# Kernel optimization log

Hardware: AMD Instinct MI355X
Metric: run time of the kernel (lower is better)

Reference implementation:

```python
import jax, jax.numpy as jnp
import numpy as np
from jax import lax

NUM_HEADS = 8
EPS = 1e-12  # torch F.normalize eps


def setup_inputs() -> dict:
    key = jax.random.key(0)
    ks = jax.random.split(key, 5)
    dim = 192
    b, h, w = 8, 128, 128
    return {
        "x": jax.random.normal(ks[0], (b, dim, h, w), jnp.float32),
        "w_qkv": jax.random.normal(ks[1], (3 * dim, dim, 1, 1), jnp.float32) * (1.0 / np.sqrt(dim)),
        "w_dw": jax.random.normal(ks[2], (3 * dim, 1, 3, 3), jnp.float32) * (1.0 / 3.0),
        "w_proj": jax.random.normal(ks[3], (dim, dim, 1, 1), jnp.float32) * (1.0 / np.sqrt(dim)),
        "temperature": jnp.ones((NUM_HEADS, 1, 1), jnp.float32),
    }


def _l2norm(t):
    n = jnp.sqrt(jnp.sum(t * t, axis=-1, keepdims=True))
    return t / jnp.maximum(n, EPS)


def reference(x, w_qkv, w_dw, w_proj, temperature):
    b, c, h, w = x.shape
    # 1x1 conv to 3*dim channels
    qkv = jnp.einsum('bchw,oc->bohw', x, w_qkv[:, :, 0, 0])
    # depthwise 3x3 conv, dilation=2, padding=2, groups=3*dim
    qkv = lax.conv_general_dilated(
        qkv, w_dw, window_strides=(1, 1), padding=((2, 2), (2, 2)),
        rhs_dilation=(2, 2), feature_group_count=3 * c,
        dimension_numbers=('NCHW', 'OIHW', 'NCHW'))
    q, k, v = jnp.split(qkv, 3, axis=1)
    ch = c // NUM_HEADS
    def heads(t):  # b (head ch) h w -> b head ch (h w)
        return t.reshape(b, NUM_HEADS, ch, h * w)
    q, k, v = heads(q), heads(k), heads(v)
    q = _l2norm(q)
    k = _l2norm(k)
    attn = jnp.einsum('bhcn,bhdn->bhcd', q, k) * temperature  # (b, head, ch, ch)
    attn = jax.nn.softmax(attn, axis=-1)
    out = jnp.einsum('bhcd,bhdn->bhcn', attn, v)
    out = out.reshape(b, c, h, w)
    out = jnp.einsum('bchw,oc->bohw', out, w_proj[:, :, 0, 0])
    return out
```

## Files before the change

### kernel.cpp

```cpp
#include <hip/hip_runtime.h>


#define DIM 192
#define NH 8
#define CH 24
#define IH 128
#define IW 128
#define NPIX (IH*IW)
#define BATCH 8
#define QKVC (3*DIM)
#define PAD 200
#define SPAD 264

typedef unsigned short u16;
typedef short bf16x8 __attribute__((ext_vector_type(8)));
typedef float f32x4 __attribute__((ext_vector_type(4)));

__device__ __forceinline__ float b2f(u16 u){
    unsigned v = ((unsigned)u) << 16;
    return __builtin_bit_cast(float, v);
}
__device__ __forceinline__ u16 f2b(float f){
    unsigned u = __builtin_bit_cast(unsigned, f);
    u += 0x7fffu + ((u >> 16) & 1u);
    return (u16)(u >> 16);
}

__device__ __forceinline__ void conv_row8(const u16* __restrict__ rp, int px0,
        float w0, float w1, float w2, float* o_){
    float f[12];
    if(px0 > 0){
        unsigned u = *(const unsigned*)(rp + px0 - 2);
        f[0] = b2f((u16)u); f[1] = b2f((u16)(u >> 16));
    } else { f[0] = 0.f; f[1] = 0.f; }
    bf16x8 v = *(const bf16x8*)(rp + px0);
    #pragma unroll
    for(int j=0;j<8;j++) f[2+j] = b2f((u16)v[j]);
    if(px0 < 120){
        unsigned u = *(const unsigned*)(rp + px0 + 8);
        f[10] = b2f((u16)u); f[11] = b2f((u16)(u >> 16));
    } else { f[10] = 0.f; f[11] = 0.f; }
    #pragma unroll
    for(int i=0;i<8;i++) o_[i] += w0*f[i] + w1*f[i+2] + w2*f[i+4];
}

__global__ __launch_bounds__(256) void k0_wcvt(const float* __restrict__ wqkv,
        u16* __restrict__ wb){
    int i = (blockIdx.x*256 + threadIdx.x)*4;
    f32x4 v = *(const f32x4*)&wqkv[i];
    unsigned lo = ((unsigned)f2b(v[1]) << 16) | f2b(v[0]);
    unsigned hi = ((unsigned)f2b(v[3]) << 16) | f2b(v[2]);
    *(uint2*)&wb[i] = make_uint2(lo, hi);
}

__global__ __launch_bounds__(256) void k1_qkv(const float* __restrict__ x,
        const u16* __restrict__ wb, u16* __restrict__ qkv_pre){
    __shared__ __align__(16) u16 Xl[64*PAD];
    const int tid = threadIdx.x;
    const int pt = blockIdx.x, b = blockIdx.y;
    const int p0 = pt*64;
    {
        const int px = tid & 63, grp = tid >> 6;
        const float* xb = x + (size_t)b*DIM*NPIX + p0 + px;
        #pragma unroll
        for(int cg = 0; cg < 6; cg++){
            int cb = grp*48 + cg*8;
            bf16x8 v;
            #pragma unroll
            for(int j=0;j<8;j++) v[j] = (short)f2b(xb[(size_t)(cb+j)*NPIX]);
            *(bf16x8*)&Xl[px*PAD + cb] = v;
        }
    }
    __syncthreads();
    const int lane = tid & 63, w = tid >> 6;
    const int r = lane & 15, quad = lane >> 4;
    u16* op = qkv_pre + (size_t)b*QKVC*NPIX + p0;
    for(int i = 0; i < 9; i++){
        const int ob = (w*9 + i)*16;
        f32x4 acc[4];
        { f32x4 z = {0.f,0.f,0.f,0.f}; for(int j=0;j<4;j++) acc[j]=z; }
        const u16* wp = wb + (size_t)(ob + r)*DIM;
        #pragma unroll
        for(int kk = 0; kk < 6; kk++){
            const int k0 = kk*32 + quad*8;
            bf16x8 a0 = *(const bf16x8*)&wp[k0];
            #pragma unroll
            for(int ni=0; ni<4; ni++){
                bf16x8 bb = *(const bf16x8*)&Xl[(ni*16 + r)*PAD + k0];
                acc[ni] = __builtin_amdgcn_mfma_f32_16x16x32_bf16(bb, a0, acc[ni], 0,0,0);
            }
        }
        #pragma unroll
        for(int ni=0; ni<4; ni++){
            int o = ob + r;
            int px = ni*16 + quad*4;
            f32x4 a = acc[ni];
            unsigned lo = ((unsigned)f2b(a[1]) << 16) | f2b(a[0]);
            unsigned hi = ((unsigned)f2b(a[3]) << 16) | f2b(a[2]);
            *(uint2*)&op[(size_t)o*NPIX + px] = make_uint2(lo, hi);
        }
    }
}

__global__ __launch_bounds__(256) void k2_gram(const u16* __restrict__ qkv_pre,
        const float* __restrict__ wdw, float* __restrict__ G){
    __shared__ __align__(16) u16 Sl[48*SPAD];
    const int tid = threadIdx.x;
    const int pc = blockIdx.x, h = blockIdx.y, b = blockIdx.z;
    const int lane = tid & 63, w = tid >> 6;
    const int r = lane & 15, quad = lane >> 4;
    f32x4 acc[6];
    { f32x4 z = {0.f,0.f,0.f,0.f}; for(int i=0;i<6;i++) acc[i]=z; }
    for(int chunk = 0; chunk < 2; chunk++){
        if(chunk) __syncthreads();
        for(int it = 0; it < 6; it++){
            int t = tid + it*256;
            int c48 = t >> 5, oct = t & 31;
            int isK = (c48 >= CH);
            int c = isK ? (c48 - CH) : c48;
            int ch = (isK ? DIM : 0) + h*CH + c;
            const u16* base = qkv_pre + ((size_t)b*QKVC + ch)*NPIX;
            const float* wv = wdw + ch*9;
            int py = pc*4 + chunk*2 + (oct >> 4);
            int px0 = (oct & 15)*8;
            float o_[8];
            #pragma unroll
            for(int i=0;i<8;i++) o_[i]=0.f;
            #pragma unroll
            for(int ky=0;ky<3;ky++){
                int ry = py + 2*ky - 2;
                if(ry < 0 || ry >= IH) continue;
                conv_row8(base + ry*IW, px0, wv[ky*3], wv[ky*3+1], wv[ky*3+2], o_);
            }
            bf16x8 v;
            #pragma unroll
            for(int i=0;i<8;i++) v[i] = (short)f2b(o_[i]);
            *(bf16x8*)&Sl[c48*SPAD + oct*8] = v;
        }
        __syncthreads();
        #pragma unroll
        for(int kk = 0; kk < 2; kk++){
            const int k0 = w*64 + kk*32 + quad*8;
            bf16x8 f0 = *(const bf16x8*)&Sl[(     r)*SPAD + k0];
            bf16x8 f1 = *(const bf16x8*)&Sl[(16 + r)*SPAD + k0];
            bf16x8 f2 = *(const bf16x8*)&Sl[(32 + r)*SPAD + k0];
            acc[0] = __builtin_amdgcn_mfma_f32_16x16x32_bf16(f0, f0, acc[0], 0,0,0);
            acc[1] = __builtin_amdgcn_mfma_f32_16x16x32_bf16(f0, f1, acc[1], 0,0,0);
            acc[2] = __builtin_amdgcn_mfma_f32_16x16x32_bf16(f0, f2, acc[2], 0,0,0);
            acc[3] = __builtin_amdgcn_mfma_f32_16x16x32_bf16(f1, f1, acc[3], 0,0,0);
            acc[4] = __builtin_amdgcn_mfma_f32_16x16x32_bf16(f1, f2, acc[4], 0,0,0);
            acc[5] = __builtin_amdgcn_mfma_f32_16x16x32_bf16(f2, f2, acc[5], 0,0,0);
        }
    }
    __syncthreads();
    float* R = (float*)Sl;
    #pragma unroll
    for(int tile=0; tile<6; tile++)
        *(f32x4*)&R[(w*6 + tile)*256 + lane*4] = acc[tile];
    __syncthreads();
    float* Gb = G + (size_t)(b*NH + h)*48*48;
    #pragma unroll
    for(int i=0; i<6; i++){
        int idx = tid + i*256;
        int tile = idx >> 8, rem = idx & 255;
        int ln = rem >> 2, t = rem & 3;
        float s = R[idx] + R[1536 + idx] + R[2*1536 + idx] + R[3*1536 + idx];
        int ti = (tile<3) ? 0 : ((tile<5) ? 1 : 2);
        int tj = (tile<3) ? tile : ((tile<5) ? (tile-2) : 2);
        int c = ti*16 + (ln >> 4)*4 + t;
        int d = tj*16 + (ln & 15);
        atomicAdd(&Gb[c*48 + d], s);
    }
}

__global__ __launch_bounds__(256) void k3_attn(const float* __restrict__ G,
        const float* __restrict__ temp, const float* __restrict__ wproj,
        u16* __restrict__ M){
    __shared__ float attn[NH][CH][CH];
    __shared__ float nq[DIM], nk[DIM];
    const int b = blockIdx.x, tid = threadIdx.x;
    const float* Gb = G + (size_t)b*NH*48*48;
    if(tid < DIM){
        int h = tid / CH, c = tid % CH;
        const float* g = Gb + (size_t)h*48*48;
        nq[tid] = fmaxf(sqrtf(g[c*48 + c]), 1e-12f);
        nk[tid] = fmaxf(sqrtf(g[(CH+c)*48 + (CH+c)]), 1e-12f);
    }
    __syncthreads();
    if(tid < DIM){
        int h = tid / CH, c = tid % CH;
        float t = temp[h];
        const float* g = Gb + (size_t)h*48*48 + c*48 + CH;
        float row[CH];
        float mx = -1e30f;
        #pragma unroll
        for(int d=0; d<CH; d++){
            float v = g[d] / (nq[tid]*nk[h*CH+d]) * t;
            row[d]=v; mx = fmaxf(mx,v);
        }
        float sum=0.f;
        #pragma unroll
        for(int d=0;d<CH;d++){ row[d]=expf(row[d]-mx); sum+=row[d]; }
        float inv = 1.f/sum;
        #pragma unroll
        for(int d=0;d<CH;d++) attn[h][c][d] = row[d]*inv;
    }
    __syncthreads();
    u16* Mb = M + (size_t)b*DIM*DIM;
    for(int i = tid; i < DIM*DIM; i += 256){
        int o = i / DIM, hd = i % DIM;
        int h = hd / CH, d = hd % CH;
        float s = 0.f;
        #pragma unroll
        for(int c=0;c<CH;c++)
            s += wproj[o*DIM + h*CH + c] * attn[h][c][d];
        Mb[i] = f2b(s);
    }
}

__global__ __launch_bounds__(256) void k45_out(const u16* __restrict__ qkv_pre,
        const float* __restrict__ wdw, const u16* __restrict__ M,
        float* __restrict__ out){
    __shared__ __align__(16) u16 Vt[64*PAD];
    const int tid = threadIdx.x;
    const int half = blockIdx.x & 1, py = blockIdx.x >> 1, b = blockIdx.y;
    const int p0 = py*IW + half*64;
    for(int it = 0; it < 3; it++){
        int t = tid + it*256;
        int chp = t >> 3, oct = t & 7;
        int px0g = half*64 + oct*8;
        float oo[2][8];
        #pragma unroll
        for(int j=0;j<2;j++){
            int ch = 2*chp + j;
            const u16* base = qkv_pre + ((size_t)b*QKVC + 2*DIM + ch)*NPIX;
            const float* wv = wdw + (2*DIM + ch)*9;
            #pragma unroll
            for(int i=0;i<8;i++) oo[j][i]=0.f;
            #pragma unroll
            for(int ky=0;ky<3;ky++){
                int ry = py + 2*ky - 2;
                if(ry < 0 || ry >= IH) continue;
                conv_row8(base + ry*IW, px0g, wv[ky*3], wv[ky*3+1], wv[ky*3+2], oo[j]);
            }
        }
        #pragma unroll
        for(int i=0;i<8;i++){
            unsigned pk = (unsigned)f2b(oo[0][i]) | ((unsigned)f2b(oo[1][i]) << 16);
            *(unsigned*)&Vt[(oct*8+i)*PAD + 2*chp] = pk;
        }
    }
    __syncthreads();
    const int lane = tid & 63, w = tid >> 6;
    const int r = lane & 15, quad = lane >> 4;
    const u16* Mb = M + (size_t)b*DIM*DIM;
    float* op = out + (size_t)b*DIM*NPIX + p0;
    for(int i = 0; i < 3; i++){
        const int ob = (w*3 + i)*16;
        f32x4 acc[4];
        { f32x4 z = {0.f,0.f,0.f,0.f}; for(int j=0;j<4;j++) acc[j]=z; }
        const u16* mp = Mb + (size_t)(ob + r)*DIM;
        #pragma unroll
        for(int kk = 0; kk < 6; kk++){
            const int k0 = kk*32 + quad*8;
            bf16x8 a0 = *(const bf16x8*)&mp[k0];
            #pragma unroll
            for(int ni=0; ni<4; ni++){
                bf16x8 bb = *(const bf16x8*)&Vt[(ni*16 + r)*PAD + k0];
                acc[ni] = __builtin_amdgcn_mfma_f32_16x16x32_bf16(bb, a0, acc[ni], 0,0,0);
            }
        }
        #pragma unroll
        for(int ni=0; ni<4; ni++)
            *(f32x4*)&op[(size_t)(ob + r)*NPIX + ni*16 + quad*4] = acc[ni];
    }
}

extern "C" void kernel_launch(void* const* d_in, const int* in_sizes, int n_in,
                              void* d_out, int out_size, void* d_ws, size_t ws_size,
                              hipStream_t stream){
    const float* x     = (const float*)d_in[0];
    const float* wqkv  = (const float*)d_in[1];
    const float* wdw   = (const float*)d_in[2];
    const float* wproj = (const float*)d_in[3];
    const float* temp  = (const float*)d_in[4];
    float* out = (float*)d_out;

    char* ws = (char*)d_ws;
    u16* qkv_pre = (u16*)ws;
    size_t off = (size_t)BATCH*QKVC*NPIX*sizeof(u16);
    float* G  = (float*)(ws + off); off += (size_t)BATCH*NH*48*48*4;
    u16* M    = (u16*)(ws + off);   off += (size_t)BATCH*DIM*DIM*2;
    u16* wb   = (u16*)(ws + off);   off += (size_t)QKVC*DIM*2;

    hipMemsetAsync(G, 0, (size_t)BATCH*NH*48*48*sizeof(float), stream);

    k0_wcvt<<<108, 256, 0, stream>>>(wqkv, wb);
    k1_qkv <<<dim3(256, BATCH), 256, 0, stream>>>(x, wb, qkv_pre);
    k2_gram<<<dim3(32, NH, BATCH), 256, 0, stream>>>(qkv_pre, wdw, G);
    k3_attn<<<BATCH, 256, 0, stream>>>(G, temp, wproj, M);
    k45_out<<<dim3(256, BATCH), 256, 0, stream>>>(qkv_pre, wdw, M, out);
}
```

Measured before the change: 446.6 us.

## Process four rows per output block with register-resident M and remapped blocks

The output kernel now runs 64 blocks per batch instead of 256, and each block loops over four image rows for one half-width. The projection matrix M fragments are loaded into registers once and reused across those rows, which removes the repeated global loads of M. Block indices in both the gram and output kernels are remapped so that neighbouring blocks work on interleaved row strips, which may change how L2 is shared between concurrent blocks. The trade-off is fewer blocks in flight (512 total on a large GPU), higher register pressure from the 18 held fragments, and a barrier for each row.

```diff
diff --git a/kernel.cpp b/kernel.cpp
--- a/kernel.cpp
+++ b/kernel.cpp
@@ -106,7 +106,8 @@
         const float* __restrict__ wdw, float* __restrict__ G){
     __shared__ __align__(16) u16 Sl[48*SPAD];
     const int tid = threadIdx.x;
-    const int pc = blockIdx.x, h = blockIdx.y, b = blockIdx.z;
+    const int bx = blockIdx.x, h = blockIdx.y, b = blockIdx.z;
+    const int pc = 4*(bx & 7) + (bx >> 3);
     const int lane = tid & 63, w = tid >> 6;
     const int r = lane & 15, quad = lane >> 4;
     f32x4 acc[6];
@@ -223,56 +224,71 @@
         float* __restrict__ out){
     __shared__ __align__(16) u16 Vt[64*PAD];
     const int tid = threadIdx.x;
-    const int half = blockIdx.x & 1, py = blockIdx.x >> 1, b = blockIdx.y;
-    const int p0 = py*IW + half*64;
-    for(int it = 0; it < 3; it++){
-        int t = tid + it*256;
-        int chp = t >> 3, oct = t & 7;
-        int px0g = half*64 + oct*8;
-        float oo[2][8];
-        #pragma unroll
-        for(int j=0;j<2;j++){
-            int ch = 2*chp + j;
-            const u16* base = qkv_pre + ((size_t)b*QKVC + 2*DIM + ch)*NPIX;
-            const float* wv = wdw + (2*DIM + ch)*9;
-            #pragma unroll
-            for(int i=0;i<8;i++) oo[j][i]=0.f;
-            #pragma unroll
-            for(int ky=0;ky<3;ky++){
-                int ry = py + 2*ky - 2;
-                if(ry < 0 || ry >= IH) continue;
-                conv_row8(base + ry*IW, px0g, wv[ky*3], wv[ky*3+1], wv[ky*3+2], oo[j]);
-            }
-        }
-        #pragma unroll
-        for(int i=0;i<8;i++){
-            unsigned pk = (unsigned)f2b(oo[0][i]) | ((unsigned)f2b(oo[1][i]) << 16);
-            *(unsigned*)&Vt[(oct*8+i)*PAD + 2*chp] = pk;
-        }
-    }
-    __syncthreads();
+    const int bx = blockIdx.x, b = blockIdx.y;
+    const int strip = 4*(bx & 7) + (bx >> 4);
+    const int half  = (bx >> 3) & 1;
+    const int r0 = strip*4;
     const int lane = tid & 63, w = tid >> 6;
     const int r = lane & 15, quad = lane >> 4;
-    const u16* Mb = M + (size_t)b*DIM*DIM;
-    float* op = out + (size_t)b*DIM*NPIX + p0;
-    for(int i = 0; i < 3; i++){
-        const int ob = (w*3 + i)*16;
-        f32x4 acc[4];
-        { f32x4 z = {0.f,0.f,0.f,0.f}; for(int j=0;j<4;j++) acc[j]=z; }
-        const u16* mp = Mb + (size_t)(ob + r)*DIM;
-        #pragma unroll
-        for(int kk = 0; kk < 6; kk++){
-            const int k0 = kk*32 + quad*8;
-            bf16x8 a0 = *(const bf16x8*)&mp[k0];
-            #pragma unroll
-            for(int ni=0; ni<4; ni++){
-                bf16x8 bb = *(const bf16x8*)&Vt[(ni*16 + r)*PAD + k0];
-                acc[ni] = __builtin_amdgcn_mfma_f32_16x16x32_bf16(bb, a0, acc[ni], 0,0,0);
-            }
-        }
-        #pragma unroll
-        for(int ni=0; ni<4; ni++)
-            *(f32x4*)&op[(size_t)(ob + r)*NPIX + ni*16 + quad*4] = acc[ni];
+    bf16x8 mreg[3][6];
+    {
+        const u16* Mb = M + (size_t)b*DIM*DIM;
+        #pragma unroll
+        for(int i=0;i<3;i++){
+            const u16* mp = Mb + (size_t)((w*3+i)*16 + r)*DIM;
+            #pragma unroll
+            for(int kk=0;kk<6;kk++)
+                mreg[i][kk] = *(const bf16x8*)&mp[kk*32 + quad*8];
+        }
+    }
+    for(int ri = 0; ri < 4; ri++){
+        const int py = r0 + ((ri & 1) << 1) + (ri >> 1);
+        if(ri) __syncthreads();
+        for(int it = 0; it < 3; it++){
+            int t = tid + it*256;
+            int chp = t >> 3, oct = t & 7;
+            int px0g = half*64 + oct*8;
+            float oo[2][8];
+            #pragma unroll
+            for(int j=0;j<2;j++){
+                int ch = 2*chp + j;
+                const u16* base = qkv_pre + ((size_t)b*QKVC + 2*DIM + ch)*NPIX;
+                const float* wv = wdw + (2*DIM + ch)*9;
+                #pragma unroll
+                for(int i=0;i<8;i++) oo[j][i]=0.f;
+                #pragma unroll
+                for(int ky=0;ky<3;ky++){
+                    int ry = py + 2*ky - 2;
+                    if(ry < 0 || ry >= IH) continue;
+                    conv_row8(base + ry*IW, px0g, wv[ky*3], wv[ky*3+1], wv[ky*3+2], oo[j]);
+                }
+            }
+            #pragma unroll
+            for(int i=0;i<8;i++){
+                unsigned pk = (unsigned)f2b(oo[0][i]) | ((unsigned)f2b(oo[1][i]) << 16);
+                *(unsigned*)&Vt[(oct*8+i)*PAD + 2*chp] = pk;
+            }
+        }
+        __syncthreads();
+        float* op = out + (size_t)b*DIM*NPIX + py*IW + half*64;
+        #pragma unroll
+        for(int i = 0; i < 3; i++){
+            const int ob = (w*3 + i)*16;
+            f32x4 acc[4];
+            { f32x4 z = {0.f,0.f,0.f,0.f}; for(int j=0;j<4;j++) acc[j]=z; }
+            #pragma unroll
+            for(int kk = 0; kk < 6; kk++){
+                const int k0 = kk*32 + quad*8;
+                #pragma unroll
+                for(int ni=0; ni<4; ni++){
+                    bf16x8 bb = *(const bf16x8*)&Vt[(ni*16 + r)*PAD + k0];
+                    acc[ni] = __builtin_amdgcn_mfma_f32_16x16x32_bf16(bb, mreg[i][kk], acc[ni], 0,0,0);
+                }
+            }
+            #pragma unroll
+            for(int ni=0; ni<4; ni++)
+                *(f32x4*)&op[(size_t)(ob + r)*NPIX + ni*16 + quad*4] = acc[ni];
+        }
     }
 }
 
@@ -299,5 +315,5 @@
     k1_qkv <<<dim3(256, BATCH), 256, 0, stream>>>(x, wb, qkv_pre);
     k2_gram<<<dim3(32, NH, BATCH), 256, 0, stream>>>(qkv_pre, wdw, G);
     k3_attn<<<BATCH, 256, 0, stream>>>(G, temp, wproj, M);
-    k45_out<<<dim3(256, BATCH), 256, 0, stream>>>(qkv_pre, wdw, M, out);
-}
+    k45_out<<<dim3(64, BATCH), 256, 0, stream>>>(qkv_pre, wdw, M, out);
+}
```

After: 431.7 us. -3.3%, faster.
